# Kernel tuning notes

Measured on AMD Instinct MI355X. Metric: run time of the kernel, lower is better.

Reference implementation:

```python
import jax, jax.numpy as jnp
import numpy as np


def dct_matrices(N):
    # torch_dct-style unnormalized DCT-II (norm=None): X_k = 2 * sum_n x_n cos(pi*(2n+1)k/(2N))
    n = jnp.arange(N, dtype=jnp.float32)
    ang = jnp.pi * (2.0 * n[None, :] + 1.0) * n[:, None] / (2.0 * N)  # [k, n]
    D = 2.0 * jnp.cos(ang)                                            # forward DCT matrix [k, n]
    w = jnp.where(n == 0, 0.5, 1.0)                                   # half-weight on DC term
    M = (jnp.cos(ang).T * w[None, :]) / (2.0 * N)                     # inverse DCT matrix [n, k]
    return D, M


def setup_inputs() -> dict:
    key = jax.random.key(0)
    k1, k2, k3 = jax.random.split(key, 3)
    B, c_in, c_out, H, W, kh, kw = 8, 64, 128, 128, 128, 5, 5
    K = float(np.sqrt(1.0 / (c_in * kh * kw)))
    x = jax.random.normal(k1, (B, c_in, H, W), dtype=jnp.float32)
    weight = (2.0 * jax.random.uniform(k2, (c_out, c_in, kh, kw), dtype=jnp.float32) - 1.0) * K
    bias = (2.0 * jax.random.uniform(k3, (c_out,), dtype=jnp.float32) - 1.0) * K
    return {"x": x, "weight": weight, "bias": bias}


def reference(x, weight, bias):
    B, c_in, H, W = x.shape
    c_out, _, kh, kw = weight.shape
    D, M = dct_matrices(H)

    # DCT-II along H axis of input
    xd = jnp.einsum('kh,bchw->bckw', D, x)            # (B, c_in, H, W)
    xf = jnp.fft.rfft(xd, axis=-1)                    # (B, c_in, H, Wf) complex

    # Pad kernel along H to full size, DCT along H, rFFT along W with n=W
    wpad = jnp.pad(weight, ((0, 0), (0, 0), (0, H - kh), (0, 0)))
    wd = jnp.einsum('kh,oihw->oikw', D, wpad)         # (c_out, c_in, H, kw)
    wf = jnp.fft.rfft(wd, n=W, axis=-1)               # (c_out, c_in, H, Wf) complex

    # Broadcast complex multiply + reduce over c_in (fused via einsum)
    hf = jnp.einsum('bchw,ochw->bohw', xf, wf)        # (B, c_out, H, Wf)
    h = jnp.fft.irfft(hf, n=W, axis=-1)               # (B, c_out, H, W)

    # Inverse DCT along H, add bias, stride slice (stride = 1)
    h = jnp.einsum('nk,bokw->bonw', M, h) + bias[None, :, None, None]
    return h[:, :, ::1, ::1]
```

## Files before the change

### kernel.cpp

```cpp
#include <hip/hip_runtime.h>


using half8v = __attribute__((ext_vector_type(8))) _Float16;
using half4v = __attribute__((ext_vector_type(4))) _Float16;
using f32x4  = __attribute__((ext_vector_type(4))) float;

#define PI_F 3.14159265358979323846f

__device__ __forceinline__ int sw_off(int n, int k, int K, int mask) {
    int c = k >> 3;
    return n * K + (((c ^ (n & mask)) << 3) | (k & 7));
}

__global__ void k_dm(_Float16* __restrict__ D, _Float16* __restrict__ M) {
    int k = blockIdx.x;
    int h = threadIdx.x;
    float ang = PI_F * (float)((2 * h + 1) * k) * (1.0f / 256.0f);
    float c = cosf(ang);
    D[k * 128 + h] = (_Float16)(2.0f * c);
    float wk = (k == 0) ? 0.5f : 1.0f;
    M[h * 128 + k] = (_Float16)(c * wk * (1.0f / 256.0f));
}

__global__ void k_wd(const float* __restrict__ w, _Float16* __restrict__ WD) {
    int bid = blockIdx.x;
    int kf = bid / 10, s = bid % 10;
    int j = s >> 1, ci0 = (s & 1) << 5;
    float dv[5];
#pragma unroll
    for (int i = 0; i < 5; ++i)
        dv[i] = 2.0f * cosf(PI_F * (float)((2 * i + 1) * kf) * (1.0f / 256.0f));
    for (int e = threadIdx.x; e < 4096; e += 256) {
        int co = e >> 5, t = e & 31, ci = ci0 + t;
        const float* wp = w + (co * 64 + ci) * 25 + j;
        float acc = 0.f;
#pragma unroll
        for (int i = 0; i < 5; ++i) acc += dv[i] * wp[i * 5];
        WD[bid * 4096 + e] = (_Float16)acc;
    }
}

__device__ __forceinline__ void gemm128(const _Float16* lA, const _Float16* lB,
                                        f32x4 acc[4][4], int tid) {
    int lane = tid & 63, ln = lane & 15, q = lane >> 4;
    int wave = tid >> 6, wm = wave >> 1, wn = wave & 1;
#pragma unroll
    for (int s = 0; s < 4; ++s) {
        half8v af[4], bf[4];
#pragma unroll
        for (int mt = 0; mt < 4; ++mt) {
            int m = wm * 64 + mt * 16 + ln;
            af[mt] = *(const half8v*)(&lA[m * 128 + (((s * 4 + q) ^ (m & 15)) << 3)]);
        }
#pragma unroll
        for (int nt = 0; nt < 4; ++nt) {
            int n = wn * 64 + nt * 16 + ln;
            bf[nt] = *(const half8v*)(&lB[n * 128 + (((s * 4 + q) ^ (n & 15)) << 3)]);
        }
#pragma unroll
        for (int mt = 0; mt < 4; ++mt)
#pragma unroll
            for (int nt = 0; nt < 4; ++nt)
                acc[mt][nt] = __builtin_amdgcn_mfma_f32_16x16x32_f16(af[mt], bf[nt], acc[mt][nt], 0, 0, 0);
    }
}

__device__ __forceinline__ void stage_copyA(const _Float16* __restrict__ g, _Float16* l, int tid) {
    const half8v* gs = (const half8v*)g;
#pragma unroll
    for (int r = 0; r < 8; ++r) {
        int gg = tid + r * 256;
        int m = gg >> 4, c = gg & 15;
        *(half8v*)(&l[m * 128 + (((c ^ (m & 15)) << 3))]) = gs[gg];
    }
}

__device__ __forceinline__ void stage_transB(const _Float16* __restrict__ src, int row_stride,
                                             _Float16* l, int K, int mask, int nblocks, int tid) {
    for (int blk = tid; blk < nblocks; blk += 256) {
        int kb = blk >> 4, wb = blk & 15;
        int k0 = kb * 4, w0 = wb * 8;
        half8v r0 = *(const half8v*)(&src[(k0 + 0) * row_stride + w0]);
        half8v r1 = *(const half8v*)(&src[(k0 + 1) * row_stride + w0]);
        half8v r2 = *(const half8v*)(&src[(k0 + 2) * row_stride + w0]);
        half8v r3 = *(const half8v*)(&src[(k0 + 3) * row_stride + w0]);
#pragma unroll
        for (int dw = 0; dw < 8; ++dw) {
            int n = w0 + dw;
            half4v p = {r0[dw], r1[dw], r2[dw], r3[dw]};
            *(half4v*)(&l[sw_off(n, k0, K, mask)]) = p;
        }
    }
}

__global__ __launch_bounds__(256) void k_dctH(const float* __restrict__ x,
                                              const _Float16* __restrict__ Dg,
                                              _Float16* __restrict__ xd) {
    __shared__ _Float16 lA[128 * 128];
    __shared__ _Float16 lB[128 * 128];
    int b = blockIdx.x >> 6, ci = blockIdx.x & 63;
    int tid = threadIdx.x;

    stage_copyA(Dg, lA, tid);

    const float* xs = x + (long)(b * 64 + ci) * 16384;
#pragma unroll
    for (int rep = 0; rep < 2; ++rep) {
        int blk = tid + rep * 256;
        int hb = blk >> 4, wb = blk & 15;
        int h0 = hb * 4, w0 = wb * 8;
        f32x4 f[4][2];
#pragma unroll
        for (int dh = 0; dh < 4; ++dh) {
            f[dh][0] = *(const f32x4*)(&xs[(h0 + dh) * 128 + w0]);
            f[dh][1] = *(const f32x4*)(&xs[(h0 + dh) * 128 + w0 + 4]);
        }
#pragma unroll
        for (int dw = 0; dw < 8; ++dw) {
            int n = w0 + dw;
            half4v p = {(_Float16)f[0][dw >> 2][dw & 3], (_Float16)f[1][dw >> 2][dw & 3],
                        (_Float16)f[2][dw >> 2][dw & 3], (_Float16)f[3][dw >> 2][dw & 3]};
            *(half4v*)(&lB[sw_off(n, h0, 128, 15)]) = p;
        }
    }
    __syncthreads();

    f32x4 acc[4][4] = {};
    gemm128(lA, lB, acc, tid);

    int lane = tid & 63, ln = lane & 15, q = lane >> 4;
    int wave = tid >> 6, wm = wave >> 1, wn = wave & 1;
#pragma unroll
    for (int mt = 0; mt < 4; ++mt)
#pragma unroll
        for (int nt = 0; nt < 4; ++nt)
#pragma unroll
            for (int r = 0; r < 4; ++r) {
                int kk = wm * 64 + mt * 16 + q * 4 + r;
                int wcol = wn * 64 + nt * 16 + ln;
                xd[((long)(kk * 8 + b) * 64 + ci) * 128 + wcol] = (_Float16)acc[mt][nt][r];
            }
}

__global__ __launch_bounds__(256) void k_conv(const _Float16* __restrict__ xd,
                                              const _Float16* __restrict__ WD,
                                              _Float16* __restrict__ y2) {
    __shared__ _Float16 lX[128 * 64];
    int bid = blockIdx.x;
    int k = bid & 127, b = bid >> 7;
    int tid = threadIdx.x;

    const _Float16* xs = xd + (long)(k * 8 + b) * 8192;
    stage_transB(xs, 128, lX, 64, 7, 256, tid);
    __syncthreads();

    int lane = tid & 63, ln = lane & 15, q = lane >> 4;
    int wave = tid >> 6, wm = wave >> 1, wn = wave & 1;
    f32x4 acc[4][4] = {};

    const _Float16* wkb = WD + (long)k * 40960;

    for (int s = 0; s < 10; ++s) {
        int j = s >> 1;
        int cb = (s & 1) << 2;
        const _Float16* wt = wkb + s * 4096;
        half8v af[4], bf[4];
#pragma unroll
        for (int mt = 0; mt < 4; ++mt) {
            int m = wm * 64 + mt * 16 + ln;
            af[mt] = *(const half8v*)(&wt[m * 32 + q * 8]);
        }
#pragma unroll
        for (int nt = 0; nt < 4; ++nt) {
            int wcol = wn * 64 + nt * 16 + ln;
            int n = (wcol - j) & 127;
            bf[nt] = *(const half8v*)(&lX[n * 64 + (((cb + q) ^ (n & 7)) << 3)]);
        }
#pragma unroll
        for (int mt = 0; mt < 4; ++mt)
#pragma unroll
            for (int nt = 0; nt < 4; ++nt)
                acc[mt][nt] = __builtin_amdgcn_mfma_f32_16x16x32_f16(af[mt], bf[nt], acc[mt][nt], 0, 0, 0);
    }

    _Float16* yb = y2 + (long)(b * 128 + k) * 16384;
#pragma unroll
    for (int mt = 0; mt < 4; ++mt)
#pragma unroll
        for (int nt = 0; nt < 4; ++nt)
#pragma unroll
            for (int r = 0; r < 4; ++r) {
                int co = wm * 64 + mt * 16 + q * 4 + r;
                int wcol = wn * 64 + nt * 16 + ln;
                yb[co * 128 + wcol] = (_Float16)acc[mt][nt][r];
            }
}

__global__ __launch_bounds__(256) void k_idct(const _Float16* __restrict__ y2,
                                              const _Float16* __restrict__ Mg,
                                              const float* __restrict__ bias,
                                              float* __restrict__ out) {
    __shared__ _Float16 lA[128 * 128];
    __shared__ _Float16 lB[128 * 128];
    int b = blockIdx.x >> 7, co = blockIdx.x & 127;
    int tid = threadIdx.x;

    stage_copyA(Mg, lA, tid);
    const _Float16* src = y2 + (long)b * 2097152 + co * 128;
    stage_transB(src, 16384, lB, 128, 15, 512, tid);
    __syncthreads();

    f32x4 acc[4][4] = {};
    gemm128(lA, lB, acc, tid);

    float bv = bias[co];
    float* ob = out + ((long)(b * 128 + co)) * 16384;
    int lane = tid & 63, ln = lane & 15, q = lane >> 4;
    int wave = tid >> 6, wm = wave >> 1, wn = wave & 1;
#pragma unroll
    for (int mt = 0; mt < 4; ++mt)
#pragma unroll
        for (int nt = 0; nt < 4; ++nt)
#pragma unroll
            for (int r = 0; r < 4; ++r) {
                int h = wm * 64 + mt * 16 + q * 4 + r;
                int wcol = wn * 64 + nt * 16 + ln;
                ob[h * 128 + wcol] = acc[mt][nt][r] + bv;
            }
}

extern "C" void kernel_launch(void* const* d_in, const int* in_sizes, int n_in,
                              void* d_out, int out_size, void* d_ws, size_t ws_size,
                              hipStream_t stream) {
    const float* x    = (const float*)d_in[0];
    const float* w    = (const float*)d_in[1];
    const float* bias = (const float*)d_in[2];
    float* out = (float*)d_out;

    char* ws = (char*)d_ws;
    _Float16* D  = (_Float16*)(ws);
    _Float16* M  = (_Float16*)(ws + 32768);
    _Float16* WD = (_Float16*)(ws + 65536);
    _Float16* xd = (_Float16*)(ws + 65536 + 10485760);
    _Float16* y2 = (_Float16*)(ws + 65536 + 10485760 + 16777216);

    k_dm  <<<dim3(128),  dim3(128), 0, stream>>>(D, M);
    k_wd  <<<dim3(1280), dim3(256), 0, stream>>>(w, WD);
    k_dctH<<<dim3(512),  dim3(256), 0, stream>>>(x, D, xd);
    k_conv<<<dim3(1024), dim3(256), 0, stream>>>(xd, WD, y2);
    k_idct<<<dim3(1024), dim3(256), 0, stream>>>(y2, M, bias, out);
}
```

Before: 159.9 us.

## Read DCT matrices directly from global memory and stage weights in LDS for k_wd

The DCT and inverse-DCT GEMM kernels no longer copy the 128x128 A matrix into shared memory. They read A fragments straight from global memory, relying on cache reuse, which halves LDS use per block and may raise occupancy. The weight-transform kernel is reorganised so each block loads one output channel's weights and a cosine table into LDS, then computes 64 frequency rows from them. This cuts redundant global reads and repeated cosine evaluation. The risk is higher global or L2 latency on the GEMM A operand inside the MFMA inner loop.

Measured after the change: 149.4 us. -6.6%, faster.

```diff
diff --git a/kernel.cpp b/kernel.cpp
--- a/kernel.cpp
+++ b/kernel.cpp
@@ -22,26 +22,35 @@
     M[h * 128 + k] = (_Float16)(c * wk * (1.0f / 256.0f));
 }
 
-__global__ void k_wd(const float* __restrict__ w, _Float16* __restrict__ WD) {
-    int bid = blockIdx.x;
-    int kf = bid / 10, s = bid % 10;
-    int j = s >> 1, ci0 = (s & 1) << 5;
-    float dv[5];
-#pragma unroll
-    for (int i = 0; i < 5; ++i)
-        dv[i] = 2.0f * cosf(PI_F * (float)((2 * i + 1) * kf) * (1.0f / 256.0f));
-    for (int e = threadIdx.x; e < 4096; e += 256) {
-        int co = e >> 5, t = e & 31, ci = ci0 + t;
-        const float* wp = w + (co * 64 + ci) * 25 + j;
+__global__ __launch_bounds__(256) void k_wd(const float* __restrict__ w, _Float16* __restrict__ WD) {
+    __shared__ float lw[1600];
+    __shared__ float lcos[320];
+    int co = blockIdx.x >> 1, k0 = (blockIdx.x & 1) << 6;
+    int tid = threadIdx.x;
+
+    for (int e = tid; e < 1600; e += 256) lw[e] = w[co * 1600 + e];
+    for (int e = tid; e < 320; e += 256) {
+        int kl = e / 5, i = e - kl * 5;
+        lcos[e] = 2.0f * cosf(PI_F * (float)((2 * i + 1) * (k0 + kl)) * (1.0f / 256.0f));
+    }
+    __syncthreads();
+
+    for (int e = tid; e < 20480; e += 256) {
+        int kk = e & 31, rest = e >> 5;
+        int s = rest % 10, kl = rest / 10;
+        int j = s >> 1, ci = ((s & 1) << 5) + kk;
+        const float* wp = &lw[ci * 25 + j];
+        const float* cp = &lcos[kl * 5];
         float acc = 0.f;
 #pragma unroll
-        for (int i = 0; i < 5; ++i) acc += dv[i] * wp[i * 5];
-        WD[bid * 4096 + e] = (_Float16)acc;
-    }
-}
-
-__device__ __forceinline__ void gemm128(const _Float16* lA, const _Float16* lB,
-                                        f32x4 acc[4][4], int tid) {
+        for (int i = 0; i < 5; ++i) acc += cp[i] * wp[i * 5];
+        WD[(((long)(k0 + kl) * 10 + s) * 128 + co) * 32 + kk] = (_Float16)acc;
+    }
+}
+
+__device__ __forceinline__ void gemm128_gA(const _Float16* __restrict__ gA,
+                                           const _Float16* lB,
+                                           f32x4 acc[4][4], int tid) {
     int lane = tid & 63, ln = lane & 15, q = lane >> 4;
     int wave = tid >> 6, wm = wave >> 1, wn = wave & 1;
 #pragma unroll
@@ -50,7 +59,7 @@
 #pragma unroll
         for (int mt = 0; mt < 4; ++mt) {
             int m = wm * 64 + mt * 16 + ln;
-            af[mt] = *(const half8v*)(&lA[m * 128 + (((s * 4 + q) ^ (m & 15)) << 3)]);
+            af[mt] = *(const half8v*)(&gA[m * 128 + (s * 4 + q) * 8]);
         }
 #pragma unroll
         for (int nt = 0; nt < 4; ++nt) {
@@ -62,16 +71,6 @@
 #pragma unroll
             for (int nt = 0; nt < 4; ++nt)
                 acc[mt][nt] = __builtin_amdgcn_mfma_f32_16x16x32_f16(af[mt], bf[nt], acc[mt][nt], 0, 0, 0);
-    }
-}
-
-__device__ __forceinline__ void stage_copyA(const _Float16* __restrict__ g, _Float16* l, int tid) {
-    const half8v* gs = (const half8v*)g;
-#pragma unroll
-    for (int r = 0; r < 8; ++r) {
-        int gg = tid + r * 256;
-        int m = gg >> 4, c = gg & 15;
-        *(half8v*)(&l[m * 128 + (((c ^ (m & 15)) << 3))]) = gs[gg];
     }
 }
 
@@ -96,12 +95,9 @@
 __global__ __launch_bounds__(256) void k_dctH(const float* __restrict__ x,
                                               const _Float16* __restrict__ Dg,
                                               _Float16* __restrict__ xd) {
-    __shared__ _Float16 lA[128 * 128];
     __shared__ _Float16 lB[128 * 128];
     int b = blockIdx.x >> 6, ci = blockIdx.x & 63;
     int tid = threadIdx.x;
-
-    stage_copyA(Dg, lA, tid);
 
     const float* xs = x + (long)(b * 64 + ci) * 16384;
 #pragma unroll
@@ -126,7 +122,7 @@
     __syncthreads();
 
     f32x4 acc[4][4] = {};
-    gemm128(lA, lB, acc, tid);
+    gemm128_gA(Dg, lB, acc, tid);
 
     int lane = tid & 63, ln = lane & 15, q = lane >> 4;
     int wave = tid >> 6, wm = wave >> 1, wn = wave & 1;
@@ -200,18 +196,16 @@
                                               const _Float16* __restrict__ Mg,
                                               const float* __restrict__ bias,
                                               float* __restrict__ out) {
-    __shared__ _Float16 lA[128 * 128];
     __shared__ _Float16 lB[128 * 128];
     int b = blockIdx.x >> 7, co = blockIdx.x & 127;
     int tid = threadIdx.x;
 
-    stage_copyA(Mg, lA, tid);
     const _Float16* src = y2 + (long)b * 2097152 + co * 128;
     stage_transB(src, 16384, lB, 128, 15, 512, tid);
     __syncthreads();
 
     f32x4 acc[4][4] = {};
-    gemm128(lA, lB, acc, tid);
+    gemm128_gA(Mg, lB, acc, tid);
 
     float bv = bias[co];
     float* ob = out + ((long)(b * 128 + co)) * 16384;
@@ -245,7 +239,7 @@
     _Float16* y2 = (_Float16*)(ws + 65536 + 10485760 + 16777216);
 
     k_dm  <<<dim3(128),  dim3(128), 0, stream>>>(D, M);
-    k_wd  <<<dim3(1280), dim3(256), 0, stream>>>(w, WD);
+    k_wd  <<<dim3(256),  dim3(256), 0, stream>>>(w, WD);
     k_dctH<<<dim3(512),  dim3(256), 0, stream>>>(x, D, xd);
     k_conv<<<dim3(1024), dim3(256), 0, stream>>>(xd, WD, y2);
     k_idct<<<dim3(1024), dim3(256), 0, stream>>>(y2, M, bias, out);
```
